# Kernel tuning notes

Hardware: AMD Instinct MI355X
Metric: run time of the kernel (lower is better)

Reference implementation:

```python
import jax, jax.numpy as jnp
import numpy as np

H = 32  # num_heads
ROPE_BASE = 10000.0


def _rope(x, offset):
    # x: [B, H, S, D]; rotate-half RoPE with position offset
    B, h, S, D = x.shape
    pos = offset + jnp.arange(S, dtype=jnp.float32)              # [S]
    inv_freq = 1.0 / (ROPE_BASE ** (jnp.arange(0, D, 2, dtype=jnp.float32) / D))  # [D/2]
    ang = pos[:, None] * inv_freq[None, :]                        # [S, D/2]
    cos = jnp.concatenate([jnp.cos(ang), jnp.cos(ang)], axis=-1)  # [S, D]
    sin = jnp.concatenate([jnp.sin(ang), jnp.sin(ang)], axis=-1)  # [S, D]
    x1, x2 = x[..., : D // 2], x[..., D // 2 :]
    rot = jnp.concatenate([-x2, x1], axis=-1)
    return x * cos + rot * sin


def setup_inputs() -> dict:
    key = jax.random.key(0)
    ks = jax.random.split(key, 8)
    B, S, HD = 8, 16, 4096
    Dh = HD // H
    PAST = 4080
    inp = {
        "x": jax.random.normal(ks[0], (B, S, HD), dtype=jnp.float32),
        "past_key": jax.random.normal(ks[1], (B, H, PAST, Dh), dtype=jnp.float32),
        "past_value": jax.random.normal(ks[2], (B, H, PAST, Dh), dtype=jnp.float32),
        "Wq": jax.random.normal(ks[3], (HD, HD), dtype=jnp.float32) * 0.02,
        "bq": jnp.zeros((HD,), dtype=jnp.float32),
        "Wk": jax.random.normal(ks[4], (HD, HD), dtype=jnp.float32) * 0.02,
        "bk": jnp.zeros((HD,), dtype=jnp.float32),
        "Wv": jax.random.normal(ks[5], (HD, HD), dtype=jnp.float32) * 0.02,
        "bv": jnp.zeros((HD,), dtype=jnp.float32),
        "Wo": jax.random.normal(ks[6], (HD, HD), dtype=jnp.float32) * 0.02,
        "bo": jnp.zeros((HD,), dtype=jnp.float32),
    }
    return inp


def reference(x, past_key, past_value, Wq, bq, Wk, bk, Wv, bv, Wo, bo):
    B, S, HD = x.shape
    Dh = HD // H
    scale = Dh ** -0.5
    past_len = past_key.shape[2]

    def split_heads(t):  # [B,S,HD] -> [B,H,S,Dh]
        return t.reshape(B, S, H, Dh).transpose(0, 2, 1, 3)

    Q = split_heads(x @ Wq.T + bq)
    K = split_heads(x @ Wk.T + bk)
    V = split_heads(x @ Wv.T + bv)

    Q = _rope(Q, past_len)
    K = _rope(K, past_len)

    K = jnp.concatenate([past_key, K], axis=2)   # [B,H,past+S,Dh]
    V = jnp.concatenate([past_value, V], axis=2)

    scores = jnp.einsum("bhqd,bhkd->bhqk", Q, K) * scale
    attn = jax.nn.softmax(scores, axis=-1)       # dropout: identity in eval
    out = jnp.einsum("bhqk,bhkd->bhqd", attn, V)
    out = out.transpose(0, 2, 1, 3).reshape(B, S, HD)
    out = out @ Wo.T + bo
    return out, attn, (K, V)
```

## Files before the change

### kernel.cpp

```cpp
#include <hip/hip_runtime.h>
#include <hip/hip_bf16.h>

#define BB 8
#define SS 16
#define HH 32
#define DH 128
#define HD 4096
#define PAST 4080
#define TOT 4096
#define MM 128

#define OUT_O  0
#define ATTN_O 524288
#define K_O    17301504
#define V_O    151519232

#define QR_O 0
#define OH_O 524288
#define STATS_O 524288
#define RT_O 1048576
#define PW_O 1050624

typedef __attribute__((ext_vector_type(8))) short short8;
typedef __attribute__((ext_vector_type(4))) float f32x4;
typedef __attribute__((ext_vector_type(4))) float f4v;

static __device__ inline unsigned short f2bf(float x) {
  __hip_bfloat16 h = __float2bfloat16(x);
  return *reinterpret_cast<unsigned short*>(&h);
}
static __device__ inline short8 cvt8(float4 a, float4 b) {
  short8 v;
  v[0] = (short)f2bf(a.x); v[1] = (short)f2bf(a.y);
  v[2] = (short)f2bf(a.z); v[3] = (short)f2bf(a.w);
  v[4] = (short)f2bf(b.x); v[5] = (short)f2bf(b.y);
  v[6] = (short)f2bf(b.z); v[7] = (short)f2bf(b.w);
  return v;
}

#define LDP 72
__global__ __launch_bounds__(256) void gemm_mfma(
    const float* __restrict__ A, const float* __restrict__ W0,
    const float* __restrict__ W1, const float* __restrict__ W2,
    float* __restrict__ P, float* __restrict__ rt) {
  if (rt != nullptr && blockIdx.x == 768) {
    int t = threadIdx.x;
#pragma unroll
    for (int i = 0; i < 4; ++i) {
      int idx = t + i * 256;
      int s = idx >> 6, j = idx & 63;
      double inv = exp(-((double)(2 * j) / 128.0) * log(10000.0));
      double ang = (double)(PAST + s) * inv;
      rt[idx] = (float)cos(ang);
      rt[1024 + idx] = (float)sin(ang);
    }
    return;
  }
  int bx = blockIdx.x;
  int mat = bx >> 8;
  int rem = bx & 255;
  int nc = rem >> 3, ks = rem & 7;
  const float* Wm = (mat == 0) ? W0 : ((mat == 1) ? W1 : W2);
  int n0 = nc * 128;
  int tid = threadIdx.x;
  int lane = tid & 63, wid = tid >> 6;
  int wm = wid >> 1, wn = wid & 1;
  int l15 = lane & 15, l4 = lane >> 4;

  __shared__ __align__(16) unsigned short As[128 * LDP];
  __shared__ __align__(16) unsigned short Bs[128 * LDP];

  f32x4 acc[4][4];
#pragma unroll
  for (int i = 0; i < 4; ++i)
#pragma unroll
    for (int j = 0; j < 4; ++j) acc[i][j] = (f32x4){0.f, 0.f, 0.f, 0.f};

  int srow = tid >> 1;
  int skh = (tid & 1) * 32;

  for (int kt = 0; kt < 8; ++kt) {
    int k0 = ks * 512 + kt * 64;
    const float* Ap = &A[(size_t)srow * 4096 + k0 + skh];
    const float* Wp = &Wm[(size_t)(n0 + srow) * 4096 + k0 + skh];
    float4 va[8], vb[8];
#pragma unroll
    for (int i = 0; i < 8; ++i) {
      va[i] = *(const float4*)(Ap + 4 * i);
      vb[i] = *(const float4*)(Wp + 4 * i);
    }
    __syncthreads();
    unsigned short* Asp = &As[srow * LDP + skh];
    unsigned short* Bsp = &Bs[srow * LDP + skh];
#pragma unroll
    for (int i = 0; i < 4; ++i) {
      *(short8*)(Asp + 8 * i) = cvt8(va[2 * i], va[2 * i + 1]);
      *(short8*)(Bsp + 8 * i) = cvt8(vb[2 * i], vb[2 * i + 1]);
    }
    __syncthreads();
#pragma unroll
    for (int s = 0; s < 2; ++s) {
      short8 af[4], bf[4];
#pragma unroll
      for (int f = 0; f < 4; ++f) {
        int ar = wm * 64 + f * 16 + l15;
        af[f] = *(const short8*)&As[ar * LDP + s * 32 + l4 * 8];
        int br = wn * 64 + f * 16 + l15;
        bf[f] = *(const short8*)&Bs[br * LDP + s * 32 + l4 * 8];
      }
#pragma unroll
      for (int i = 0; i < 4; ++i)
#pragma unroll
        for (int j = 0; j < 4; ++j)
          acc[i][j] = __builtin_amdgcn_mfma_f32_16x16x32_bf16(
              af[i], bf[j], acc[i][j], 0, 0, 0);
    }
  }

  float* Pb = P + (size_t)(mat * 8 + ks) * 524288 + n0;
#pragma unroll
  for (int i = 0; i < 4; ++i) {
#pragma unroll
    for (int j = 0; j < 4; ++j) {
      int mbase = wm * 64 + i * 16 + l4 * 4;
      int nn = wn * 64 + j * 16 + l15;
#pragma unroll
      for (int r = 0; r < 4; ++r)
        Pb[(size_t)(mbase + r) * 4096 + nn] = acc[i][j][r];
    }
  }
}

__global__ __launch_bounds__(256) void qkv_reduce(
    const float* __restrict__ P, const float* __restrict__ bq,
    const float* __restrict__ bk, const float* __restrict__ bv,
    const float* __restrict__ rt, float* __restrict__ qr,
    float* __restrict__ kout, float* __restrict__ vout) {
  int t = blockIdx.x * 256 + threadIdx.x;
  int d2 = t & 63;
  int h = (t >> 6) & 31;
  int m = (t >> 11) & 127;
  int mat = t >> 18;
  int n1 = h * 128 + d2, n2 = n1 + 64;
  const float* bias = (mat == 0) ? bq : ((mat == 1) ? bk : bv);
  float v1 = bias[n1], v2 = bias[n2];
  const float* Pm = P + (size_t)(mat * 8) * 524288 + (size_t)m * 4096;
#pragma unroll
  for (int s = 0; s < 8; ++s) {
    v1 += Pm[(size_t)s * 524288 + n1];
    v2 += Pm[(size_t)s * 524288 + n2];
  }
  int st = m & 15, b = m >> 4;
  int bh = b * 32 + h;
  if (mat == 2) {
    size_t dst = (size_t)(bh * TOT + PAST + st) * 128;
    vout[dst + d2] = v1; vout[dst + 64 + d2] = v2;
  } else {
    float c = rt[st * 64 + d2], sn = rt[1024 + st * 64 + d2];
    float o1 = v1 * c - v2 * sn;
    float o2 = v2 * c + v1 * sn;
    if (mat == 0) {
      size_t dst = (size_t)(bh * 16 + st) * 128;
      qr[dst + d2] = o1; qr[dst + 64 + d2] = o2;
    } else {
      size_t dst = (size_t)(bh * TOT + PAST + st) * 128;
      kout[dst + d2] = o1; kout[dst + 64 + d2] = o2;
    }
  }
}

#define KST 136
__global__ __launch_bounds__(256) void scores_mfma(
    const float* __restrict__ pastk, const float* __restrict__ qr,
    float* __restrict__ kout, float* __restrict__ attn,
    float* __restrict__ stats) {
  int bh = blockIdx.x >> 5, kc = blockIdx.x & 31;
  int r0 = kc * 128;
  int tid = threadIdx.x, lane = tid & 63, w = tid >> 6;
  int l15 = lane & 15, l4 = lane >> 4;

  __shared__ __align__(16) unsigned short Ks[128 * KST];
  __shared__ __align__(16) unsigned short Qs[16 * KST];
  __shared__ float sred[2][4][16];

  const f4v* pk4 = (const f4v*)pastk;
  f4v* ko4 = (f4v*)kout;

#pragma unroll
  for (int i = 0; i < 16; ++i) {
    int f = tid + i * 256;
    int row = f >> 5, c = f & 31;
    int grow = r0 + row;
    size_t kidx = (size_t)(bh * TOT + grow) * 32 + c;
    f4v v;
    if (grow < PAST) {
      v = __builtin_nontemporal_load(pk4 + ((size_t)(bh * PAST + grow) * 32 + c));
      __builtin_nontemporal_store(v, ko4 + kidx);
    } else {
      v = *((const f4v*)ko4 + kidx);
    }
    ushort4 u;
    u.x = f2bf(v.x); u.y = f2bf(v.y); u.z = f2bf(v.z); u.w = f2bf(v.w);
    *(ushort4*)&Ks[row * KST + c * 4] = u;
  }
#pragma unroll
  for (int i = 0; i < 2; ++i) {
    int f = tid + i * 256;
    int q = f >> 5, c = f & 31;
    f4v v = *(const f4v*)&qr[(size_t)bh * 2048 + q * 128 + c * 4];
    ushort4 u;
    u.x = f2bf(v.x); u.y = f2bf(v.y); u.z = f2bf(v.z); u.w = f2bf(v.w);
    *(ushort4*)&Qs[q * KST + c * 4] = u;
  }
  __syncthreads();

  f32x4 acc0 = (f32x4){0.f, 0.f, 0.f, 0.f};
  f32x4 acc1 = (f32x4){0.f, 0.f, 0.f, 0.f};
#pragma unroll
  for (int s = 0; s < 4; ++s) {
    short8 aq = *(const short8*)&Qs[l15 * KST + s * 32 + l4 * 8];
    short8 b0 = *(const short8*)&Ks[(w * 32 + l15) * KST + s * 32 + l4 * 8];
    short8 b1 = *(const short8*)&Ks[(w * 32 + 16 + l15) * KST + s * 32 + l4 * 8];
    acc0 = __builtin_amdgcn_mfma_f32_16x16x32_bf16(aq, b0, acc0, 0, 0, 0);
    acc1 = __builtin_amdgcn_mfma_f32_16x16x32_bf16(aq, b1, acc1, 0, 0, 0);
  }
  const float scale = 0.088388347648318447f;
  float v0[4], v1[4], mx[4], ex[4];
#pragma unroll
  for (int r = 0; r < 4; ++r) {
    v0[r] = acc0[r] * scale;
    v1[r] = acc1[r] * scale;
    int q = l4 * 4 + r;
    size_t base = (size_t)(bh * 16 + q) * 4096 + r0 + w * 32 + l15;
    attn[base] = v0[r];
    attn[base + 16] = v1[r];
    mx[r] = fmaxf(v0[r], v1[r]);
  }
#pragma unroll
  for (int r = 0; r < 4; ++r) {
#pragma unroll
    for (int off = 1; off < 16; off <<= 1)
      mx[r] = fmaxf(mx[r], __shfl_xor(mx[r], off));
    ex[r] = __expf(v0[r] - mx[r]) + __expf(v1[r] - mx[r]);
#pragma unroll
    for (int off = 1; off < 16; off <<= 1)
      ex[r] += __shfl_xor(ex[r], off);
  }
  if (l15 == 0) {
#pragma unroll
    for (int r = 0; r < 4; ++r) {
      sred[0][w][l4 * 4 + r] = mx[r];
      sred[1][w][l4 * 4 + r] = ex[r];
    }
  }
  __syncthreads();
  if (tid < 16) {
    float M = sred[0][0][tid];
#pragma unroll
    for (int ww = 1; ww < 4; ++ww) M = fmaxf(M, sred[0][ww][tid]);
    float E = 0.f;
#pragma unroll
    for (int ww = 0; ww < 4; ++ww)
      E += sred[1][ww][tid] * __expf(sred[0][ww][tid] - M);
    size_t si = ((size_t)(bh * 16 + tid) * 32 + kc) * 2;
    stats[si] = M; stats[si + 1] = E;
  }
}

__global__ __launch_bounds__(256) void pv_kernel(
    const float* __restrict__ pastv, float* __restrict__ attn,
    const float* __restrict__ stats, float* __restrict__ vout,
    float* __restrict__ pvp) {
  int blk = blockIdx.x;
  int bh = blk >> 3, nc = blk & 7;
  int tid = threadIdx.x;
  int dq = tid & 31, rg = tid >> 5;
  __shared__ __align__(16) float red[4][16][128];
  float* atn = &red[0][0][0];
  __shared__ float sm[16], si[16];

  {
    int row = tid >> 4, c0 = (tid & 15) * 2;
    float4 s4 = *(const float4*)&stats[((size_t)(bh * 16 + row) * 32 + c0) * 2];
    float m = fmaxf(s4.x, s4.z);
    float e = s4.y * __expf(s4.x - m) + s4.w * __expf(s4.z - m);
#pragma unroll
    for (int off = 1; off < 16; off <<= 1) {
      float mo = __shfl_xor(m, off), eo = __shfl_xor(e, off);
      float M = fmaxf(m, mo);
      e = e * __expf(m - M) + eo * __expf(mo - M);
      m = M;
    }
    if ((tid & 15) == 0) { sm[row] = m; si[row] = 1.f / e; }
  }
  float acc[16][4];
#pragma unroll
  for (int q = 0; q < 16; ++q)
#pragma unroll
    for (int j = 0; j < 4; ++j) acc[q][j] = 0.f;

  const f4v* pv4 = (const f4v*)pastv;
  f4v* vo4 = (f4v*)vout;
  int base0 = nc * 512;
  __syncthreads();

  for (int slab = 0; slab < 4; ++slab) {
    int kbase = base0 + slab * 128;
#pragma unroll
    for (int i = 0; i < 8; ++i) {
      int idx = tid + i * 256;
      int q = idx >> 7, k = idx & 127;
      size_t ai = (size_t)(bh * 16 + q) * 4096 + kbase + k;
      float p = __expf(attn[ai] - sm[q]) * si[q];
      atn[q * 128 + k] = p;
      __builtin_nontemporal_store(p, &attn[ai]);
    }
    __syncthreads();
#pragma unroll 2
    for (int it = 0; it < 16; it += 2) {
      int kk0 = it * 8 + rg, kk1 = kk0 + 8;
      int row0 = kbase + kk0, row1 = kbase + kk1;
      size_t o0 = (size_t)(bh * TOT + row0) * 32 + dq;
      size_t o1 = (size_t)(bh * TOT + row1) * 32 + dq;
      const f4v* s0 = (row0 < PAST)
          ? (pv4 + ((size_t)(bh * PAST + row0) * 32 + dq)) : (const f4v*)(vo4 + o0);
      const f4v* s1 = (row1 < PAST)
          ? (pv4 + ((size_t)(bh * PAST + row1) * 32 + dq)) : (const f4v*)(vo4 + o1);
      f4v x0 = __builtin_nontemporal_load(s0);
      f4v x1 = __builtin_nontemporal_load(s1);
      if (row0 < PAST) __builtin_nontemporal_store(x0, vo4 + o0);
      if (row1 < PAST) __builtin_nontemporal_store(x1, vo4 + o1);
#pragma unroll
      for (int q = 0; q < 16; ++q) {
        float a = atn[q * 128 + kk0];
        acc[q][0] = fmaf(a, x0.x, acc[q][0]);
        acc[q][1] = fmaf(a, x0.y, acc[q][1]);
        acc[q][2] = fmaf(a, x0.z, acc[q][2]);
        acc[q][3] = fmaf(a, x0.w, acc[q][3]);
      }
#pragma unroll
      for (int q = 0; q < 16; ++q) {
        float a = atn[q * 128 + kk1];
        acc[q][0] = fmaf(a, x1.x, acc[q][0]);
        acc[q][1] = fmaf(a, x1.y, acc[q][1]);
        acc[q][2] = fmaf(a, x1.z, acc[q][2]);
        acc[q][3] = fmaf(a, x1.w, acc[q][3]);
      }
    }
    __syncthreads();
  }
#pragma unroll
  for (int q = 0; q < 16; ++q)
#pragma unroll
    for (int j = 0; j < 4; ++j) acc[q][j] += __shfl_xor(acc[q][j], 32);
  int wid = tid >> 6;
  if ((tid & 63) < 32) {
#pragma unroll
    for (int q = 0; q < 16; ++q) {
      f4v o; o.x = acc[q][0]; o.y = acc[q][1]; o.z = acc[q][2]; o.w = acc[q][3];
      *(f4v*)&red[wid][q][dq * 4] = o;
    }
  }
  __syncthreads();
#pragma unroll
  for (int rep = 0; rep < 8; ++rep) {
    int o = tid + rep * 256;
    int q = o >> 7, dd = o & 127;
    float s = red[0][q][dd] + red[1][q][dd] + red[2][q][dd] + red[3][q][dd];
    pvp[((size_t)(bh * 8 + nc) * 16 + q) * 128 + dd] = s;
  }
}

__global__ __launch_bounds__(256) void pv_reduce(
    const float* __restrict__ pvp, float* __restrict__ oh) {
  int t = blockIdx.x * 256 + threadIdx.x;
  int dd = t & 127;
  int q = (t >> 7) & 15;
  int bh = t >> 11;
  int b = bh >> 5, h = bh & 31;
  float s = 0.f;
#pragma unroll
  for (int nc = 0; nc < 8; ++nc)
    s += pvp[((size_t)(bh * 8 + nc) * 16 + q) * 128 + dd];
  oh[(size_t)(b * 16 + q) * 4096 + h * 128 + dd] = s;
}

__global__ __launch_bounds__(256) void out_reduce(
    const float* __restrict__ P, const float* __restrict__ bo,
    float* __restrict__ out) {
  int t = blockIdx.x * 256 + threadIdx.x;
  float v = bo[t & 4095];
#pragma unroll
  for (int s = 0; s < 8; ++s) v += P[(size_t)s * 524288 + t];
  out[t] = v;
}

extern "C" void kernel_launch(void* const* d_in, const int* in_sizes, int n_in,
                              void* d_out, int out_size, void* d_ws, size_t ws_size,
                              hipStream_t stream) {
  const float* x     = (const float*)d_in[0];
  const float* pastk = (const float*)d_in[1];
  const float* pastv = (const float*)d_in[2];
  const float* Wq = (const float*)d_in[3];
  const float* bq = (const float*)d_in[4];
  const float* Wk = (const float*)d_in[5];
  const float* bk = (const float*)d_in[6];
  const float* Wv = (const float*)d_in[7];
  const float* bv = (const float*)d_in[8];
  const float* Wo = (const float*)d_in[9];
  const float* bo = (const float*)d_in[10];

  float* out  = (float*)d_out;
  float* attn = out + ATTN_O;
  float* kout = out + K_O;
  float* vout = out + V_O;

  float* ws = (float*)d_ws;
  float* qr    = ws + QR_O;
  float* oh    = ws + OH_O;
  float* stats = ws + STATS_O;
  float* rt    = ws + RT_O;
  float* pw    = ws + PW_O;

  gemm_mfma<<<769, 256, 0, stream>>>(x, Wq, Wk, Wv, attn, rt);
  qkv_reduce<<<3072, 256, 0, stream>>>(attn, bq, bk, bv, rt, qr, kout, vout);
  scores_mfma<<<8192, 256, 0, stream>>>(pastk, qr, kout, attn, stats);
  pv_kernel<<<2048, 256, 0, stream>>>(pastv, attn, stats, vout, pw);
  pv_reduce<<<2048, 256, 0, stream>>>(pw, oh);
  gemm_mfma<<<256, 256, 0, stream>>>(oh, Wo, Wo, Wo, pw, nullptr);
  out_reduce<<<2048, 256, 0, stream>>>(pw, bo, out);
}
```

Before: 607.0 us.

## Fuse QKV projection with bias and RoPE into direct kernel; halve PV splits

Replaces the split-K QKV GEMM plus reduce kernel with a single kernel that computes full-K tiles per head chunk and applies bias and RoPE in the epilogue, computing sin/cos inline instead of from a precomputed table. This removes the partial-sum write/read traffic and one launch. Separately, the PV kernel now processes 1024 keys per block with 4 splits instead of 8, reducing partial outputs at the cost of fewer blocks. The new QKV kernel has only 384 blocks with a long serial K loop and small tiles, which may underutilize the GPU. The float sinf on large angles may also be less accurate than the old double-precision table.

After: 644.3 us. 1.06x slower.

```diff
diff --git a/kernel.cpp b/kernel.cpp
--- a/kernel.cpp
+++ b/kernel.cpp
@@ -18,7 +18,6 @@
 #define QR_O 0
 #define OH_O 524288
 #define STATS_O 524288
-#define RT_O 1048576
 #define PW_O 1050624
 
 typedef __attribute__((ext_vector_type(8))) short short8;
@@ -38,29 +37,105 @@
   return v;
 }
 
+__global__ __launch_bounds__(256) void qkv_direct(
+    const float* __restrict__ x,
+    const float* __restrict__ Wq, const float* __restrict__ bq,
+    const float* __restrict__ Wk, const float* __restrict__ bk,
+    const float* __restrict__ Wv, const float* __restrict__ bv,
+    float* __restrict__ qr, float* __restrict__ kout, float* __restrict__ vout) {
+  int bx = blockIdx.x;
+  int mat = bx >> 7;
+  int rem = bx & 127;
+  int h = rem >> 2, c = rem & 3;
+  const float* Wm = (mat == 0) ? Wq : ((mat == 1) ? Wk : Wv);
+  const float* bias = (mat == 0) ? bq : ((mat == 1) ? bk : bv);
+  int tid = threadIdx.x, lane = tid & 63, w = tid >> 6;
+  int l15 = lane & 15, l4 = lane >> 4;
+
+  __shared__ __align__(16) unsigned short As[128 * 72];
+  __shared__ __align__(16) unsigned short Ws[32 * 72];
+
+  f32x4 acc[2][2];
+#pragma unroll
+  for (int i = 0; i < 2; ++i)
+#pragma unroll
+    for (int j = 0; j < 2; ++j) acc[i][j] = (f32x4){0.f, 0.f, 0.f, 0.f};
+
+  int arow = tid >> 1, aoff = (tid & 1) * 32;
+  int wrow = tid >> 3, wcol = (tid & 7) * 8;
+  int wgrow = h * 128 + c * 16 + (wrow < 16 ? wrow : 48 + wrow);
+  const float* Ap = &x[(size_t)arow * 4096 + aoff];
+  const float* Wp = &Wm[(size_t)wgrow * 4096 + wcol];
+
+  for (int kt = 0; kt < 64; ++kt) {
+    int k0 = kt * 64;
+    float4 va[8];
+#pragma unroll
+    for (int i = 0; i < 8; ++i) va[i] = *(const float4*)(Ap + k0 + 4 * i);
+    f4v vw0 = __builtin_nontemporal_load((const f4v*)(Wp + k0));
+    f4v vw1 = __builtin_nontemporal_load((const f4v*)(Wp + k0 + 4));
+    __syncthreads();
+    unsigned short* Asp = &As[arow * 72 + aoff];
+#pragma unroll
+    for (int i = 0; i < 4; ++i)
+      *(short8*)(Asp + 8 * i) = cvt8(va[2 * i], va[2 * i + 1]);
+    float4 w0 = {vw0.x, vw0.y, vw0.z, vw0.w};
+    float4 w1 = {vw1.x, vw1.y, vw1.z, vw1.w};
+    *(short8*)&Ws[wrow * 72 + wcol] = cvt8(w0, w1);
+    __syncthreads();
+#pragma unroll
+    for (int s = 0; s < 2; ++s) {
+      short8 a0 = *(const short8*)&As[(w * 32 + l15) * 72 + s * 32 + l4 * 8];
+      short8 a1 = *(const short8*)&As[(w * 32 + 16 + l15) * 72 + s * 32 + l4 * 8];
+      short8 b0 = *(const short8*)&Ws[l15 * 72 + s * 32 + l4 * 8];
+      short8 b1 = *(const short8*)&Ws[(16 + l15) * 72 + s * 32 + l4 * 8];
+      acc[0][0] = __builtin_amdgcn_mfma_f32_16x16x32_bf16(a0, b0, acc[0][0], 0, 0, 0);
+      acc[0][1] = __builtin_amdgcn_mfma_f32_16x16x32_bf16(a0, b1, acc[0][1], 0, 0, 0);
+      acc[1][0] = __builtin_amdgcn_mfma_f32_16x16x32_bf16(a1, b0, acc[1][0], 0, 0, 0);
+      acc[1][1] = __builtin_amdgcn_mfma_f32_16x16x32_bf16(a1, b1, acc[1][1], 0, 0, 0);
+    }
+  }
+
+  int col_lo = c * 16 + l15;
+  float blo = bias[h * 128 + col_lo];
+  float bhi = bias[h * 128 + col_lo + 64];
+  float inv = exp2f((float)col_lo * -0.20762051f);
+#pragma unroll
+  for (int i = 0; i < 2; ++i) {
+#pragma unroll
+    for (int r = 0; r < 4; ++r) {
+      int m = w * 32 + i * 16 + l4 * 4 + r;
+      int b = m >> 4, st = m & 15;
+      int bh = b * 32 + h;
+      float v1 = acc[i][0][r] + blo;
+      float v2 = acc[i][1][r] + bhi;
+      if (mat == 2) {
+        size_t dst = (size_t)(bh * TOT + PAST + st) * 128 + col_lo;
+        vout[dst] = v1; vout[dst + 64] = v2;
+      } else {
+        float ang = (float)(PAST + st) * inv;
+        float sn = sinf(ang), cs = cosf(ang);
+        float o1 = v1 * cs - v2 * sn;
+        float o2 = v2 * cs + v1 * sn;
+        if (mat == 0) {
+          size_t dst = (size_t)(bh * 16 + st) * 128 + col_lo;
+          qr[dst] = o1; qr[dst + 64] = o2;
+        } else {
+          size_t dst = (size_t)(bh * TOT + PAST + st) * 128 + col_lo;
+          kout[dst] = o1; kout[dst + 64] = o2;
+        }
+      }
+    }
+  }
+}
+
 #define LDP 72
 __global__ __launch_bounds__(256) void gemm_mfma(
     const float* __restrict__ A, const float* __restrict__ W0,
-    const float* __restrict__ W1, const float* __restrict__ W2,
-    float* __restrict__ P, float* __restrict__ rt) {
-  if (rt != nullptr && blockIdx.x == 768) {
-    int t = threadIdx.x;
-#pragma unroll
-    for (int i = 0; i < 4; ++i) {
-      int idx = t + i * 256;
-      int s = idx >> 6, j = idx & 63;
-      double inv = exp(-((double)(2 * j) / 128.0) * log(10000.0));
-      double ang = (double)(PAST + s) * inv;
-      rt[idx] = (float)cos(ang);
-      rt[1024 + idx] = (float)sin(ang);
-    }
-    return;
-  }
+    float* __restrict__ P) {
   int bx = blockIdx.x;
-  int mat = bx >> 8;
-  int rem = bx & 255;
-  int nc = rem >> 3, ks = rem & 7;
-  const float* Wm = (mat == 0) ? W0 : ((mat == 1) ? W1 : W2);
+  int nc = bx >> 3, ks = bx & 7;
+  const float* Wm = W0;
   int n0 = nc * 128;
   int tid = threadIdx.x;
   int lane = tid & 63, wid = tid >> 6;
@@ -117,7 +192,7 @@
     }
   }
 
-  float* Pb = P + (size_t)(mat * 8 + ks) * 524288 + n0;
+  float* Pb = P + (size_t)ks * 524288 + n0;
 #pragma unroll
   for (int i = 0; i < 4; ++i) {
 #pragma unroll
@@ -127,44 +202,6 @@
 #pragma unroll
       for (int r = 0; r < 4; ++r)
         Pb[(size_t)(mbase + r) * 4096 + nn] = acc[i][j][r];
-    }
-  }
-}
-
-__global__ __launch_bounds__(256) void qkv_reduce(
-    const float* __restrict__ P, const float* __restrict__ bq,
-    const float* __restrict__ bk, const float* __restrict__ bv,
-    const float* __restrict__ rt, float* __restrict__ qr,
-    float* __restrict__ kout, float* __restrict__ vout) {
-  int t = blockIdx.x * 256 + threadIdx.x;
-  int d2 = t & 63;
-  int h = (t >> 6) & 31;
-  int m = (t >> 11) & 127;
-  int mat = t >> 18;
-  int n1 = h * 128 + d2, n2 = n1 + 64;
-  const float* bias = (mat == 0) ? bq : ((mat == 1) ? bk : bv);
-  float v1 = bias[n1], v2 = bias[n2];
-  const float* Pm = P + (size_t)(mat * 8) * 524288 + (size_t)m * 4096;
-#pragma unroll
-  for (int s = 0; s < 8; ++s) {
-    v1 += Pm[(size_t)s * 524288 + n1];
-    v2 += Pm[(size_t)s * 524288 + n2];
-  }
-  int st = m & 15, b = m >> 4;
-  int bh = b * 32 + h;
-  if (mat == 2) {
-    size_t dst = (size_t)(bh * TOT + PAST + st) * 128;
-    vout[dst + d2] = v1; vout[dst + 64 + d2] = v2;
-  } else {
-    float c = rt[st * 64 + d2], sn = rt[1024 + st * 64 + d2];
-    float o1 = v1 * c - v2 * sn;
-    float o2 = v2 * c + v1 * sn;
-    if (mat == 0) {
-      size_t dst = (size_t)(bh * 16 + st) * 128;
-      qr[dst + d2] = o1; qr[dst + 64 + d2] = o2;
-    } else {
-      size_t dst = (size_t)(bh * TOT + PAST + st) * 128;
-      kout[dst + d2] = o1; kout[dst + 64 + d2] = o2;
     }
   }
 }
@@ -272,7 +309,7 @@
     const float* __restrict__ stats, float* __restrict__ vout,
     float* __restrict__ pvp) {
   int blk = blockIdx.x;
-  int bh = blk >> 3, nc = blk & 7;
+  int bh = blk >> 2, nc = blk & 3;
   int tid = threadIdx.x;
   int dq = tid & 31, rg = tid >> 5;
   __shared__ __align__(16) float red[4][16][128];
@@ -301,10 +338,10 @@
 
   const f4v* pv4 = (const f4v*)pastv;
   f4v* vo4 = (f4v*)vout;
-  int base0 = nc * 512;
+  int base0 = nc * 1024;
   __syncthreads();
 
-  for (int slab = 0; slab < 4; ++slab) {
+  for (int slab = 0; slab < 8; ++slab) {
     int kbase = base0 + slab * 128;
 #pragma unroll
     for (int i = 0; i < 8; ++i) {
@@ -367,7 +404,7 @@
     int o = tid + rep * 256;
     int q = o >> 7, dd = o & 127;
     float s = red[0][q][dd] + red[1][q][dd] + red[2][q][dd] + red[3][q][dd];
-    pvp[((size_t)(bh * 8 + nc) * 16 + q) * 128 + dd] = s;
+    pvp[((size_t)(bh * 4 + nc) * 16 + q) * 128 + dd] = s;
   }
 }
 
@@ -380,8 +417,8 @@
   int b = bh >> 5, h = bh & 31;
   float s = 0.f;
 #pragma unroll
-  for (int nc = 0; nc < 8; ++nc)
-    s += pvp[((size_t)(bh * 8 + nc) * 16 + q) * 128 + dd];
+  for (int nc = 0; nc < 4; ++nc)
+    s += pvp[((size_t)(bh * 4 + nc) * 16 + q) * 128 + dd];
   oh[(size_t)(b * 16 + q) * 4096 + h * 128 + dd] = s;
 }
 
@@ -419,14 +456,12 @@
   float* qr    = ws + QR_O;
   float* oh    = ws + OH_O;
   float* stats = ws + STATS_O;
-  float* rt    = ws + RT_O;
   float* pw    = ws + PW_O;
 
-  gemm_mfma<<<769, 256, 0, stream>>>(x, Wq, Wk, Wv, attn, rt);
-  qkv_reduce<<<3072, 256, 0, stream>>>(attn, bq, bk, bv, rt, qr, kout, vout);
+  qkv_direct<<<384, 256, 0, stream>>>(x, Wq, bq, Wk, bk, Wv, bv, qr, kout, vout);
   scores_mfma<<<8192, 256, 0, stream>>>(pastk, qr, kout, attn, stats);
-  pv_kernel<<<2048, 256, 0, stream>>>(pastv, attn, stats, vout, pw);
+  pv_kernel<<<1024, 256, 0, stream>>>(pastv, attn, stats, vout, pw);
   pv_reduce<<<2048, 256, 0, stream>>>(pw, oh);
-  gemm_mfma<<<256, 256, 0, stream>>>(oh, Wo, Wo, Wo, pw, nullptr);
+  gemm_mfma<<<256, 256, 0, stream>>>(oh, Wo, pw);
   out_reduce<<<2048, 256, 0, stream>>>(pw, bo, out);
 }
```
